# Kernel tuning notes

Hardware: AMD Instinct MI355X
Metric: run time of the kernel (lower is better)

Reference implementation:

```python
import jax, jax.numpy as jnp
import numpy as np

N = 100000
E = 1600000
IN_C, HID_C, OUT_C = 512, 256, 64
K = 10
ALPHA = 0.1


def setup_inputs() -> dict:
    key = jax.random.key(0)
    k1, k2, k3, k4 = jax.random.split(key, 4)
    x = jax.random.normal(k1, (N, IN_C), dtype=jnp.float32)
    edge_index = jax.random.randint(k2, (2, E), 0, N, dtype=jnp.int64)
    # Glorot-ish scaled linear weights
    W1 = jax.random.normal(k3, (HID_C, IN_C), dtype=jnp.float32) / np.sqrt(IN_C)
    b1 = jnp.zeros((HID_C,), dtype=jnp.float32)
    W2 = jax.random.normal(k4, (OUT_C, HID_C), dtype=jnp.float32) / np.sqrt(HID_C)
    b2 = jnp.zeros((OUT_C,), dtype=jnp.float32)
    # PPR init: temp[k] = alpha*(1-alpha)^k, temp[K] = (1-alpha)^K
    temp = ALPHA * (1.0 - ALPHA) ** np.arange(K + 1)
    temp[-1] = (1.0 - ALPHA) ** K
    temp = jnp.asarray(temp, dtype=jnp.float32)
    return {"x": x, "edge_index": edge_index, "W1": W1, "b1": b1,
            "W2": W2, "b2": b2, "temp": temp}


def _gcn_norm(edge_index, num_nodes):
    # add self loops with weight 1, symmetric normalization D^-1/2 A D^-1/2
    loop = jnp.arange(num_nodes, dtype=edge_index.dtype)
    src = jnp.concatenate([edge_index[0], loop])
    dst = jnp.concatenate([edge_index[1], loop])
    w = jnp.ones(src.shape[0], dtype=jnp.float32)
    deg = jax.ops.segment_sum(w, dst, num_segments=num_nodes)
    dinv = jnp.where(deg > 0, jax.lax.rsqrt(deg), 0.0)
    norm = dinv[src] * w * dinv[dst]
    return src, dst, norm


def reference(x, edge_index, W1, b1, W2, b2, temp):
    # MLP (inference mode: dropout is identity)
    h = jax.nn.relu(x @ W1.T + b1)
    h = h @ W2.T + b2  # [N, OUT_C]

    src, dst, norm = _gcn_norm(edge_index, N)
    norm = norm[:, None]

    def step(carry, gamma):
        xk, hidden = carry
        xk = jax.ops.segment_sum(norm * xk[src], dst, num_segments=N)
        hidden = hidden + gamma * xk
        return (xk, hidden), None

    hidden0 = temp[0] * h
    (_, hidden), _ = jax.lax.scan(step, (h, hidden0), temp[1:])
    return hidden
```

## Files before the change

### kernel.cpp

```cpp
#include <hip/hip_runtime.h>

#define IN_C   512
#define HID_C  256
#define OUT_C  64
#define KSTEPS 10

typedef __attribute__((ext_vector_type(8))) short bf16x8;
typedef __attribute__((ext_vector_type(4))) float f32x4;

__device__ __forceinline__ uint f2bf(float f) {
    uint u = __float_as_uint(f);
    return (u + 0x7fffu + ((u >> 16) & 1u)) >> 16;
}
__device__ __forceinline__ float bfl(uint u) { return __uint_as_float(u << 16); }
__device__ __forceinline__ float bfh(uint u) { return __uint_as_float(u & 0xffff0000u); }

__global__ void k_init(int* __restrict__ a, int* __restrict__ b, int n) {
    int i = blockIdx.x * blockDim.x + threadIdx.x;
    if (i < n) { a[i] = 0; b[i] = 0; }
}

__global__ void k_hist(const int* __restrict__ ei, int* __restrict__ cnt, int E) {
    int e = blockIdx.x * blockDim.x + threadIdx.x;
    if (e < E) atomicAdd(&cnt[ei[E + e]], 1);
}

__global__ void k_dinv(const int* __restrict__ cnt, float* __restrict__ dinv, int n) {
    int i = blockIdx.x * blockDim.x + threadIdx.x;
    if (i < n) dinv[i] = rsqrtf((float)cnt[i] + 1.0f);
}

__global__ void k_scan1(const int* __restrict__ cnt, int* __restrict__ ptr,
                        int* __restrict__ bsum, int n) {
    __shared__ int sh[256];
    int i = blockIdx.x * 256 + threadIdx.x;
    int v = (i < n) ? cnt[i] : 0;
    sh[threadIdx.x] = v;
    __syncthreads();
    for (int off = 1; off < 256; off <<= 1) {
        int t = (threadIdx.x >= off) ? sh[threadIdx.x - off] : 0;
        __syncthreads();
        sh[threadIdx.x] += t;
        __syncthreads();
    }
    if (i < n) ptr[i + 1] = sh[threadIdx.x];
    if (threadIdx.x == 255) bsum[blockIdx.x] = sh[255];
}

__global__ void k_scan2(int* __restrict__ bsum, int nb) {
    __shared__ int sh[512];
    int t = threadIdx.x;
    int v = (t < nb) ? bsum[t] : 0;
    sh[t] = v;
    __syncthreads();
    for (int off = 1; off < 512; off <<= 1) {
        int u = (t >= off) ? sh[t - off] : 0;
        __syncthreads();
        sh[t] += u;
        __syncthreads();
    }
    int ex = (t == 0) ? 0 : sh[t - 1];
    if (t < nb) bsum[t] = ex;
}

__global__ void k_scan3(int* __restrict__ ptr, const int* __restrict__ bsum, int n) {
    int i = blockIdx.x * blockDim.x + threadIdx.x;
    if (i < n) ptr[i + 1] += bsum[i >> 8];
    if (i == 0) ptr[0] = 0;
}

__global__ void k_scatter(const int* __restrict__ ei, const float* __restrict__ dinv,
                          const int* __restrict__ rowptr, int* __restrict__ fill,
                          int2* __restrict__ edges, int E) {
    int e = blockIdx.x * blockDim.x + threadIdx.x;
    if (e < E) {
        int s = ei[e], d = ei[E + e];
        float nv = dinv[s] * dinv[d];
        int pos = rowptr[d] + atomicAdd(&fill[d], 1);
        edges[pos] = make_int2(s, __float_as_int(nv));
    }
}

__global__ void k_cvtw1(const float* __restrict__ W1, ushort* __restrict__ w1kt) {
    int i = blockIdx.x * blockDim.x + threadIdx.x;
    if (i < HID_C * IN_C) {
        int o = i >> 9;
        int c = i & 511;
        int kb = c >> 3, j = c & 7;
        w1kt[((size_t)kb * HID_C + o) * 8 + j] = (ushort)f2bf(W1[i]);
    }
}

__global__ void k_cvtw2(const float* __restrict__ W2, ushort* __restrict__ w2kt) {
    int i = blockIdx.x * blockDim.x + threadIdx.x;
    if (i < OUT_C * HID_C) {
        int o = i >> 8, c = i & 255;
        int kb = c >> 3, j = c & 7;
        w2kt[((size_t)(kb * 64 + o)) * 8 + j] = (ushort)f2bf(W2[i]);
    }
}

__global__ __launch_bounds__(256, 4) void k_mlp(
    const float* __restrict__ x, const ushort* __restrict__ w1kt,
    const float* __restrict__ b1, const ushort* __restrict__ w2kt,
    const float* __restrict__ b2, const float* __restrict__ temp,
    ushort* __restrict__ h, float* __restrict__ out, int n)
{
    __shared__ uint4 smem4[2048];
    char* smem = (char*)smem4;

    const int tid = threadIdx.x;
    const int lane = tid & 63;
    const int w    = tid >> 6;
    const int l15  = lane & 15;
    const int l4   = lane >> 4;
    const int row0 = blockIdx.x * 64;

    f32x4 acc[4][4];
#pragma unroll
    for (int i = 0; i < 4; ++i)
#pragma unroll
        for (int j = 0; j < 4; ++j) acc[i][j] = (f32x4){0.f, 0.f, 0.f, 0.f};

    for (int k0 = 0; k0 < IN_C; k0 += 64) {
#pragma unroll
        for (int it = 0; it < 4; ++it) {
            int f  = tid + it * 256;
            int r  = f >> 4, c4 = f & 15;
            int gr = row0 + r; if (gr >= n) gr = n - 1;
            float4 v = *(const float4*)(x + (size_t)gr * IN_C + k0 + c4 * 4);
            uint p0 = f2bf(v.x) | (f2bf(v.y) << 16);
            uint p1 = f2bf(v.z) | (f2bf(v.w) << 16);
            int boff = (c4 * 8) ^ ((r & 7) << 4);
            *(uint2*)(smem + r * 128 + boff) = make_uint2(p0, p1);
        }
        __syncthreads();

#pragma unroll
        for (int kk = 0; kk < 2; ++kk) {
            bf16x8 af[4], bfr[4];
            int kb = kk * 4 + l4;
#pragma unroll
            for (int rf = 0; rf < 4; ++rf) {
                int r = rf * 16 + l15;
                af[rf] = *(const bf16x8*)(smem + r * 128 + ((kb ^ (r & 7)) << 4));
            }
            int kbg = (k0 >> 3) + kb;
#pragma unroll
            for (int nf = 0; nf < 4; ++nf) {
                int nn = w * 64 + nf * 16 + l15;
                bfr[nf] = *(const bf16x8*)(w1kt + ((size_t)kbg * HID_C + nn) * 8);
            }
#pragma unroll
            for (int rf = 0; rf < 4; ++rf)
#pragma unroll
                for (int nf = 0; nf < 4; ++nf)
                    acc[rf][nf] = __builtin_amdgcn_mfma_f32_16x16x32_bf16(
                        af[rf], bfr[nf], acc[rf][nf], 0, 0, 0);
        }
        __syncthreads();
    }

    float bias1[4];
#pragma unroll
    for (int nf = 0; nf < 4; ++nf) bias1[nf] = b1[w * 64 + nf * 16 + l15];
#pragma unroll
    for (int rf = 0; rf < 4; ++rf)
#pragma unroll
        for (int nf = 0; nf < 4; ++nf)
#pragma unroll
            for (int j = 0; j < 4; ++j) {
                int r = rf * 16 + l4 * 4 + j;
                int c = w * 64 + nf * 16 + l15;
                float v = fmaxf(acc[rf][nf][j] + bias1[nf], 0.f);
                int byte = r * 512 + ((((c >> 3) ^ (r & 7))) << 4) + (c & 7) * 2;
                *(ushort*)(smem + byte) = (ushort)f2bf(v);
            }
    __syncthreads();

    f32x4 acc2[4];
#pragma unroll
    for (int nf = 0; nf < 4; ++nf) acc2[nf] = (f32x4){0.f, 0.f, 0.f, 0.f};
#pragma unroll
    for (int kk = 0; kk < 8; ++kk) {
        int r = w * 16 + l15;
        int kb = kk * 4 + l4;
        bf16x8 a = *(const bf16x8*)(smem + r * 512 + ((kb ^ (r & 7)) << 4));
#pragma unroll
        for (int nf = 0; nf < 4; ++nf) {
            bf16x8 bb = *(const bf16x8*)(w2kt + ((size_t)kb * 64 + nf * 16 + l15) * 8);
            acc2[nf] = __builtin_amdgcn_mfma_f32_16x16x32_bf16(a, bb, acc2[nf], 0, 0, 0);
        }
    }

    float t0 = temp[0];
#pragma unroll
    for (int nf = 0; nf < 4; ++nf) {
        int c = nf * 16 + l15;
        float bias = b2[c];
#pragma unroll
        for (int j = 0; j < 4; ++j) {
            int gr = row0 + w * 16 + l4 * 4 + j;
            if (gr < n) {
                float v = acc2[nf][j] + bias;
                h[(size_t)gr * OUT_C + c]   = (ushort)f2bf(v);
                out[(size_t)gr * OUT_C + c] = t0 * v;
            }
        }
    }
}

__global__ __launch_bounds__(256) void k_prop(
    const int* __restrict__ rowptr, const int2* __restrict__ edges,
    const ushort* __restrict__ cur, ushort* __restrict__ nxt,
    float* __restrict__ out, const float* __restrict__ dinv,
    const float* __restrict__ temp, int kcur, int do_rmw, int do_nxt, int n)
{
    const int lane = threadIdx.x & 63;
    const int g    = lane >> 3;
    const int sl   = lane & 7;
    const int wid  = (blockIdx.x * blockDim.x + threadIdx.x) >> 6;
    const int nw   = (gridDim.x * blockDim.x) >> 6;
    const float gc = temp[kcur];
    const float gp = temp[kcur - 1];

    for (int base = wid * 8; base < n; base += nw * 8) {
        int d = base + g;
        bool act = d < n;
        int dd = act ? d : (n - 1);
        int b = rowptr[dd];
        int en = act ? rowptr[dd + 1] : b;
        float di = dinv[dd];
        size_t rowoff = (size_t)dd * OUT_C + sl * 8;

        uint4 sraw = *(const uint4*)(cur + rowoff);
        float c0 = bfl(sraw.x), c1 = bfh(sraw.x), c2 = bfl(sraw.y), c3 = bfh(sraw.y),
              c4 = bfl(sraw.z), c5 = bfh(sraw.z), c6 = bfl(sraw.w), c7 = bfh(sraw.w);
        float s = di * di;
        float a0 = s * c0, a1 = s * c1, a2 = s * c2, a3 = s * c3,
              a4 = s * c4, a5 = s * c5, a6 = s * c6, a7 = s * c7;

        int i = b;
        for (; i + 4 <= en; i += 4) {
            int2 e0 = edges[i], e1 = edges[i + 1], e2 = edges[i + 2], e3 = edges[i + 3];
            uint4 r0 = *(const uint4*)(cur + (size_t)e0.x * OUT_C + sl * 8);
            uint4 r1 = *(const uint4*)(cur + (size_t)e1.x * OUT_C + sl * 8);
            uint4 r2 = *(const uint4*)(cur + (size_t)e2.x * OUT_C + sl * 8);
            uint4 r3 = *(const uint4*)(cur + (size_t)e3.x * OUT_C + sl * 8);
            float w0 = __int_as_float(e0.y), w1 = __int_as_float(e1.y);
            float w2 = __int_as_float(e2.y), w3 = __int_as_float(e3.y);
            a0 = fmaf(w0, bfl(r0.x), a0); a1 = fmaf(w0, bfh(r0.x), a1);
            a2 = fmaf(w0, bfl(r0.y), a2); a3 = fmaf(w0, bfh(r0.y), a3);
            a4 = fmaf(w0, bfl(r0.z), a4); a5 = fmaf(w0, bfh(r0.z), a5);
            a6 = fmaf(w0, bfl(r0.w), a6); a7 = fmaf(w0, bfh(r0.w), a7);
            a0 = fmaf(w1, bfl(r1.x), a0); a1 = fmaf(w1, bfh(r1.x), a1);
            a2 = fmaf(w1, bfl(r1.y), a2); a3 = fmaf(w1, bfh(r1.y), a3);
            a4 = fmaf(w1, bfl(r1.z), a4); a5 = fmaf(w1, bfh(r1.z), a5);
            a6 = fmaf(w1, bfl(r1.w), a6); a7 = fmaf(w1, bfh(r1.w), a7);
            a0 = fmaf(w2, bfl(r2.x), a0); a1 = fmaf(w2, bfh(r2.x), a1);
            a2 = fmaf(w2, bfl(r2.y), a2); a3 = fmaf(w2, bfh(r2.y), a3);
            a4 = fmaf(w2, bfl(r2.z), a4); a5 = fmaf(w2, bfh(r2.z), a5);
            a6 = fmaf(w2, bfl(r2.w), a6); a7 = fmaf(w2, bfh(r2.w), a7);
            a0 = fmaf(w3, bfl(r3.x), a0); a1 = fmaf(w3, bfh(r3.x), a1);
            a2 = fmaf(w3, bfl(r3.y), a2); a3 = fmaf(w3, bfh(r3.y), a3);
            a4 = fmaf(w3, bfl(r3.z), a4); a5 = fmaf(w3, bfh(r3.z), a5);
            a6 = fmaf(w3, bfl(r3.w), a6); a7 = fmaf(w3, bfh(r3.w), a7);
        }
        for (; i < en; ++i) {
            int2 e = edges[i];
            uint4 r0 = *(const uint4*)(cur + (size_t)e.x * OUT_C + sl * 8);
            float w0 = __int_as_float(e.y);
            a0 = fmaf(w0, bfl(r0.x), a0); a1 = fmaf(w0, bfh(r0.x), a1);
            a2 = fmaf(w0, bfl(r0.y), a2); a3 = fmaf(w0, bfh(r0.y), a3);
            a4 = fmaf(w0, bfl(r0.z), a4); a5 = fmaf(w0, bfh(r0.z), a5);
            a6 = fmaf(w0, bfl(r0.w), a6); a7 = fmaf(w0, bfh(r0.w), a7);
        }

        if (act) {
            if (do_nxt) {
                uint4 pk;
                pk.x = f2bf(a0) | (f2bf(a1) << 16);
                pk.y = f2bf(a2) | (f2bf(a3) << 16);
                pk.z = f2bf(a4) | (f2bf(a5) << 16);
                pk.w = f2bf(a6) | (f2bf(a7) << 16);
                *(uint4*)(nxt + rowoff) = pk;
            }
            if (do_rmw) {
                float4* op = (float4*)(out + rowoff);
                float4 v0 = op[0], v1 = op[1];
                v0.x += gp * c0 + gc * a0; v0.y += gp * c1 + gc * a1;
                v0.z += gp * c2 + gc * a2; v0.w += gp * c3 + gc * a3;
                v1.x += gp * c4 + gc * a4; v1.y += gp * c5 + gc * a5;
                v1.z += gp * c6 + gc * a6; v1.w += gp * c7 + gc * a7;
                op[0] = v0; op[1] = v1;
            }
        }
    }
}

extern "C" void kernel_launch(void* const* d_in, const int* in_sizes, int n_in,
                              void* d_out, int out_size, void* d_ws, size_t ws_size,
                              hipStream_t stream)
{
    const float* x    = (const float*)d_in[0];
    const int*   ei   = (const int*)d_in[1];
    const float* W1   = (const float*)d_in[2];
    const float* b1   = (const float*)d_in[3];
    const float* W2   = (const float*)d_in[4];
    const float* b2   = (const float*)d_in[5];
    const float* temp = (const float*)d_in[6];
    float* out = (float*)d_out;

    const int N = in_sizes[0] / IN_C;
    const int E = in_sizes[1] / 2;

    char* ws = (char*)d_ws;
    ushort* bufA  = (ushort*)ws;
    ushort* bufB  = bufA + (size_t)N * OUT_C;
    int2*   edges = (int2*)(bufB + (size_t)N * OUT_C);
    ushort* w1kt  = (ushort*)(edges + E);
    ushort* w2kt  = w1kt + HID_C * IN_C;
    float*  dinv  = (float*)(w2kt + OUT_C * HID_C);
    int*    cnt    = (int*)(dinv + N);
    int*    fill   = cnt + N;
    int*    rowptr = fill + N;
    int*    bsum   = rowptr + (N + 16);

    const int nbN = (N + 255) / 256;
    const int nbE = (E + 255) / 256;

    k_init   <<<nbN, 256, 0, stream>>>(cnt, fill, N);
    k_hist   <<<nbE, 256, 0, stream>>>(ei, cnt, E);
    k_dinv   <<<nbN, 256, 0, stream>>>(cnt, dinv, N);
    k_scan1  <<<nbN, 256, 0, stream>>>(cnt, rowptr, bsum, N);
    k_scan2  <<<1,   512, 0, stream>>>(bsum, nbN);
    k_scan3  <<<nbN, 256, 0, stream>>>(rowptr, bsum, N);
    k_scatter<<<nbE, 256, 0, stream>>>(ei, dinv, rowptr, fill, edges, E);
    k_cvtw1  <<<(HID_C * IN_C + 255) / 256, 256, 0, stream>>>(W1, w1kt);
    k_cvtw2  <<<(OUT_C * HID_C + 255) / 256, 256, 0, stream>>>(W2, w2kt);

    k_mlp<<<(N + 63) / 64, 256, 0, stream>>>(x, w1kt, b1, w2kt, b2, temp, bufA, out, N);

    ushort* cur = bufA;
    ushort* nxt = bufB;
    for (int k = 1; k <= KSTEPS; ++k) {
        int do_rmw = (k % 2 == 0) ? 1 : 0;
        int do_nxt = (k < KSTEPS) ? 1 : 0;
        k_prop<<<2048, 256, 0, stream>>>(rowptr, edges, cur, nxt, out, dinv,
                                         temp, k, do_rmw, do_nxt, N);
        ushort* t = cur; cur = nxt; nxt = t;
    }
}
```

Measured before the change: 589.7 us.

## Split feature matrix into four 16-column planes to shrink gather working set

The MLP output is stored as four column planes of 16 bf16 features each, and the propagation kernel walks the planes one at a time so each gather touches a 3.2MB plane instead of the full 12.8MB matrix, aiming for better cache hit rates on random neighbor reads. Each node is now handled by 4 lanes loading 8 bytes apiece, and the grid grows to one block per 64 nodes. In exchange, CSR row pointers and edge lists are read four times per step, each gather moves only 8 bytes per lane, and the out read-modify-write is split into strided 16-byte pieces.

```diff
diff --git a/kernel.cpp b/kernel.cpp
--- a/kernel.cpp
+++ b/kernel.cpp
@@ -115,6 +115,7 @@
     const int l15  = lane & 15;
     const int l4   = lane >> 4;
     const int row0 = blockIdx.x * 64;
+    const size_t plane = (size_t)n * 16;
 
     f32x4 acc[4][4];
 #pragma unroll
@@ -203,7 +204,7 @@
             int gr = row0 + w * 16 + l4 * 4 + j;
             if (gr < n) {
                 float v = acc2[nf][j] + bias;
-                h[(size_t)gr * OUT_C + c]   = (ushort)f2bf(v);
+                h[(size_t)nf * plane + (size_t)gr * 16 + l15] = (ushort)f2bf(v);
                 out[(size_t)gr * OUT_C + c] = t0 * v;
             }
         }
@@ -217,82 +218,66 @@
     const float* __restrict__ temp, int kcur, int do_rmw, int do_nxt, int n)
 {
     const int lane = threadIdx.x & 63;
-    const int g    = lane >> 3;
-    const int sl   = lane & 7;
+    const int g    = lane >> 2;
+    const int q    = lane & 3;
     const int wid  = (blockIdx.x * blockDim.x + threadIdx.x) >> 6;
     const int nw   = (gridDim.x * blockDim.x) >> 6;
     const float gc = temp[kcur];
     const float gp = temp[kcur - 1];
-
-    for (int base = wid * 8; base < n; base += nw * 8) {
-        int d = base + g;
-        bool act = d < n;
-        int dd = act ? d : (n - 1);
-        int b = rowptr[dd];
-        int en = act ? rowptr[dd + 1] : b;
-        float di = dinv[dd];
-        size_t rowoff = (size_t)dd * OUT_C + sl * 8;
-
-        uint4 sraw = *(const uint4*)(cur + rowoff);
-        float c0 = bfl(sraw.x), c1 = bfh(sraw.x), c2 = bfl(sraw.y), c3 = bfh(sraw.y),
-              c4 = bfl(sraw.z), c5 = bfh(sraw.z), c6 = bfl(sraw.w), c7 = bfh(sraw.w);
-        float s = di * di;
-        float a0 = s * c0, a1 = s * c1, a2 = s * c2, a3 = s * c3,
-              a4 = s * c4, a5 = s * c5, a6 = s * c6, a7 = s * c7;
-
-        int i = b;
-        for (; i + 4 <= en; i += 4) {
-            int2 e0 = edges[i], e1 = edges[i + 1], e2 = edges[i + 2], e3 = edges[i + 3];
-            uint4 r0 = *(const uint4*)(cur + (size_t)e0.x * OUT_C + sl * 8);
-            uint4 r1 = *(const uint4*)(cur + (size_t)e1.x * OUT_C + sl * 8);
-            uint4 r2 = *(const uint4*)(cur + (size_t)e2.x * OUT_C + sl * 8);
-            uint4 r3 = *(const uint4*)(cur + (size_t)e3.x * OUT_C + sl * 8);
-            float w0 = __int_as_float(e0.y), w1 = __int_as_float(e1.y);
-            float w2 = __int_as_float(e2.y), w3 = __int_as_float(e3.y);
-            a0 = fmaf(w0, bfl(r0.x), a0); a1 = fmaf(w0, bfh(r0.x), a1);
-            a2 = fmaf(w0, bfl(r0.y), a2); a3 = fmaf(w0, bfh(r0.y), a3);
-            a4 = fmaf(w0, bfl(r0.z), a4); a5 = fmaf(w0, bfh(r0.z), a5);
-            a6 = fmaf(w0, bfl(r0.w), a6); a7 = fmaf(w0, bfh(r0.w), a7);
-            a0 = fmaf(w1, bfl(r1.x), a0); a1 = fmaf(w1, bfh(r1.x), a1);
-            a2 = fmaf(w1, bfl(r1.y), a2); a3 = fmaf(w1, bfh(r1.y), a3);
-            a4 = fmaf(w1, bfl(r1.z), a4); a5 = fmaf(w1, bfh(r1.z), a5);
-            a6 = fmaf(w1, bfl(r1.w), a6); a7 = fmaf(w1, bfh(r1.w), a7);
-            a0 = fmaf(w2, bfl(r2.x), a0); a1 = fmaf(w2, bfh(r2.x), a1);
-            a2 = fmaf(w2, bfl(r2.y), a2); a3 = fmaf(w2, bfh(r2.y), a3);
-            a4 = fmaf(w2, bfl(r2.z), a4); a5 = fmaf(w2, bfh(r2.z), a5);
-            a6 = fmaf(w2, bfl(r2.w), a6); a7 = fmaf(w2, bfh(r2.w), a7);
-            a0 = fmaf(w3, bfl(r3.x), a0); a1 = fmaf(w3, bfh(r3.x), a1);
-            a2 = fmaf(w3, bfl(r3.y), a2); a3 = fmaf(w3, bfh(r3.y), a3);
-            a4 = fmaf(w3, bfl(r3.z), a4); a5 = fmaf(w3, bfh(r3.z), a5);
-            a6 = fmaf(w3, bfl(r3.w), a6); a7 = fmaf(w3, bfh(r3.w), a7);
-        }
-        for (; i < en; ++i) {
-            int2 e = edges[i];
-            uint4 r0 = *(const uint4*)(cur + (size_t)e.x * OUT_C + sl * 8);
-            float w0 = __int_as_float(e.y);
-            a0 = fmaf(w0, bfl(r0.x), a0); a1 = fmaf(w0, bfh(r0.x), a1);
-            a2 = fmaf(w0, bfl(r0.y), a2); a3 = fmaf(w0, bfh(r0.y), a3);
-            a4 = fmaf(w0, bfl(r0.z), a4); a5 = fmaf(w0, bfh(r0.z), a5);
-            a6 = fmaf(w0, bfl(r0.w), a6); a7 = fmaf(w0, bfh(r0.w), a7);
-        }
-
-        if (act) {
-            if (do_nxt) {
-                uint4 pk;
-                pk.x = f2bf(a0) | (f2bf(a1) << 16);
-                pk.y = f2bf(a2) | (f2bf(a3) << 16);
-                pk.z = f2bf(a4) | (f2bf(a5) << 16);
-                pk.w = f2bf(a6) | (f2bf(a7) << 16);
-                *(uint4*)(nxt + rowoff) = pk;
-            }
-            if (do_rmw) {
-                float4* op = (float4*)(out + rowoff);
-                float4 v0 = op[0], v1 = op[1];
-                v0.x += gp * c0 + gc * a0; v0.y += gp * c1 + gc * a1;
-                v0.z += gp * c2 + gc * a2; v0.w += gp * c3 + gc * a3;
-                v1.x += gp * c4 + gc * a4; v1.y += gp * c5 + gc * a5;
-                v1.z += gp * c6 + gc * a6; v1.w += gp * c7 + gc * a7;
-                op[0] = v0; op[1] = v1;
+    const size_t plane = (size_t)n * 16;
+
+    for (int p = 0; p < 4; ++p) {
+        const ushort* curp = cur + (size_t)p * plane;
+        ushort*       nxtp = nxt + (size_t)p * plane;
+
+        for (int base = wid * 16; base < n; base += nw * 16) {
+            int d = base + g;
+            bool act = d < n;
+            int dd = act ? d : (n - 1);
+            int b = rowptr[dd];
+            int en = act ? rowptr[dd + 1] : b;
+            float di = dinv[dd];
+            size_t ro = (size_t)dd * 16 + q * 4;
+
+            uint2 sraw = *(const uint2*)(curp + ro);
+            float c0 = bfl(sraw.x), c1 = bfh(sraw.x);
+            float c2 = bfl(sraw.y), c3 = bfh(sraw.y);
+            float s = di * di;
+            float a0 = s * c0, a1 = s * c1, a2 = s * c2, a3 = s * c3;
+
+            int i = b;
+            for (; i + 2 <= en; i += 2) {
+                int2 e0 = edges[i], e1 = edges[i + 1];
+                uint2 r0 = *(const uint2*)(curp + (size_t)e0.x * 16 + q * 4);
+                uint2 r1 = *(const uint2*)(curp + (size_t)e1.x * 16 + q * 4);
+                float w0 = __int_as_float(e0.y), w1 = __int_as_float(e1.y);
+                a0 = fmaf(w0, bfl(r0.x), a0); a1 = fmaf(w0, bfh(r0.x), a1);
+                a2 = fmaf(w0, bfl(r0.y), a2); a3 = fmaf(w0, bfh(r0.y), a3);
+                a0 = fmaf(w1, bfl(r1.x), a0); a1 = fmaf(w1, bfh(r1.x), a1);
+                a2 = fmaf(w1, bfl(r1.y), a2); a3 = fmaf(w1, bfh(r1.y), a3);
+            }
+            if (i < en) {
+                int2 e0 = edges[i];
+                uint2 r0 = *(const uint2*)(curp + (size_t)e0.x * 16 + q * 4);
+                float w0 = __int_as_float(e0.y);
+                a0 = fmaf(w0, bfl(r0.x), a0); a1 = fmaf(w0, bfh(r0.x), a1);
+                a2 = fmaf(w0, bfl(r0.y), a2); a3 = fmaf(w0, bfh(r0.y), a3);
+            }
+
+            if (act) {
+                if (do_nxt) {
+                    uint2 pk;
+                    pk.x = f2bf(a0) | (f2bf(a1) << 16);
+                    pk.y = f2bf(a2) | (f2bf(a3) << 16);
+                    *(uint2*)(nxtp + ro) = pk;
+                }
+                if (do_rmw) {
+                    float4* op = (float4*)(out + (size_t)dd * OUT_C + p * 16 + q * 4);
+                    float4 v = op[0];
+                    v.x += gp * c0 + gc * a0; v.y += gp * c1 + gc * a1;
+                    v.z += gp * c2 + gc * a2; v.w += gp * c3 + gc * a3;
+                    op[0] = v;
+                }
             }
         }
     }
@@ -328,6 +313,7 @@
 
     const int nbN = (N + 255) / 256;
     const int nbE = (E + 255) / 256;
+    const int nbP = (N + 63) / 64;
 
     k_init   <<<nbN, 256, 0, stream>>>(cnt, fill, N);
     k_hist   <<<nbE, 256, 0, stream>>>(ei, cnt, E);
@@ -346,8 +332,8 @@
     for (int k = 1; k <= KSTEPS; ++k) {
         int do_rmw = (k % 2 == 0) ? 1 : 0;
         int do_nxt = (k < KSTEPS) ? 1 : 0;
-        k_prop<<<2048, 256, 0, stream>>>(rowptr, edges, cur, nxt, out, dinv,
-                                         temp, k, do_rmw, do_nxt, N);
+        k_prop<<<nbP, 256, 0, stream>>>(rowptr, edges, cur, nxt, out, dinv,
+                                        temp, k, do_rmw, do_nxt, N);
         ushort* t = cur; cur = nxt; nxt = t;
     }
 }
```

Result: slower. 993.2 us (+68.4%).

## Sort destination nodes by degree and launch one 8-lane group per node

Applied to the files above, without the earlier changes.

Adds a small counting sort that buckets nodes by in-degree, capped at 63, into a permutation array. The propagation kernel then gives each 8-lane group exactly one node taken from that permutation, with a grid sized to cover all nodes instead of a fixed 2048-block grid-stride loop. The aim is to cut load imbalance inside a wavefront, since the 8 groups in a wave now have similar edge counts. In exchange, rows are visited in permuted order, so writes to nxt and out lose their coalescing and locality, and three extra setup kernels run.

```diff
diff --git a/kernel.cpp b/kernel.cpp
--- a/kernel.cpp
+++ b/kernel.cpp
@@ -81,6 +81,28 @@
     }
 }
 
+__global__ void k_dhist(const int* __restrict__ cnt, int* __restrict__ dh, int n) {
+    int i = blockIdx.x * blockDim.x + threadIdx.x;
+    if (i < n) atomicAdd(&dh[min(cnt[i], 63)], 1);
+}
+
+__global__ void k_dscan(int* __restrict__ dh) {
+    if (threadIdx.x == 0) {
+        int acc = 0;
+        for (int b = 0; b < 64; ++b) { int v = dh[b]; dh[b] = acc; acc += v; }
+    }
+}
+
+__global__ void k_dscat(const int* __restrict__ cnt, const int* __restrict__ dh,
+                        int* __restrict__ dfill, int* __restrict__ perm, int n) {
+    int i = blockIdx.x * blockDim.x + threadIdx.x;
+    if (i < n) {
+        int b = min(cnt[i], 63);
+        int pos = dh[b] + atomicAdd(&dfill[b], 1);
+        perm[pos] = i;
+    }
+}
+
 __global__ void k_cvtw1(const float* __restrict__ W1, ushort* __restrict__ w1kt) {
     int i = blockIdx.x * blockDim.x + threadIdx.x;
     if (i < HID_C * IN_C) {
@@ -212,6 +234,7 @@
 
 __global__ __launch_bounds__(256) void k_prop(
     const int* __restrict__ rowptr, const int2* __restrict__ edges,
+    const int* __restrict__ perm,
     const ushort* __restrict__ cur, ushort* __restrict__ nxt,
     float* __restrict__ out, const float* __restrict__ dinv,
     const float* __restrict__ temp, int kcur, int do_rmw, int do_nxt, int n)
@@ -220,80 +243,77 @@
     const int g    = lane >> 3;
     const int sl   = lane & 7;
     const int wid  = (blockIdx.x * blockDim.x + threadIdx.x) >> 6;
-    const int nw   = (gridDim.x * blockDim.x) >> 6;
     const float gc = temp[kcur];
     const float gp = temp[kcur - 1];
 
-    for (int base = wid * 8; base < n; base += nw * 8) {
-        int d = base + g;
-        bool act = d < n;
-        int dd = act ? d : (n - 1);
-        int b = rowptr[dd];
-        int en = act ? rowptr[dd + 1] : b;
-        float di = dinv[dd];
-        size_t rowoff = (size_t)dd * OUT_C + sl * 8;
-
-        uint4 sraw = *(const uint4*)(cur + rowoff);
-        float c0 = bfl(sraw.x), c1 = bfh(sraw.x), c2 = bfl(sraw.y), c3 = bfh(sraw.y),
-              c4 = bfl(sraw.z), c5 = bfh(sraw.z), c6 = bfl(sraw.w), c7 = bfh(sraw.w);
-        float s = di * di;
-        float a0 = s * c0, a1 = s * c1, a2 = s * c2, a3 = s * c3,
-              a4 = s * c4, a5 = s * c5, a6 = s * c6, a7 = s * c7;
-
-        int i = b;
-        for (; i + 4 <= en; i += 4) {
-            int2 e0 = edges[i], e1 = edges[i + 1], e2 = edges[i + 2], e3 = edges[i + 3];
-            uint4 r0 = *(const uint4*)(cur + (size_t)e0.x * OUT_C + sl * 8);
-            uint4 r1 = *(const uint4*)(cur + (size_t)e1.x * OUT_C + sl * 8);
-            uint4 r2 = *(const uint4*)(cur + (size_t)e2.x * OUT_C + sl * 8);
-            uint4 r3 = *(const uint4*)(cur + (size_t)e3.x * OUT_C + sl * 8);
-            float w0 = __int_as_float(e0.y), w1 = __int_as_float(e1.y);
-            float w2 = __int_as_float(e2.y), w3 = __int_as_float(e3.y);
-            a0 = fmaf(w0, bfl(r0.x), a0); a1 = fmaf(w0, bfh(r0.x), a1);
-            a2 = fmaf(w0, bfl(r0.y), a2); a3 = fmaf(w0, bfh(r0.y), a3);
-            a4 = fmaf(w0, bfl(r0.z), a4); a5 = fmaf(w0, bfh(r0.z), a5);
-            a6 = fmaf(w0, bfl(r0.w), a6); a7 = fmaf(w0, bfh(r0.w), a7);
-            a0 = fmaf(w1, bfl(r1.x), a0); a1 = fmaf(w1, bfh(r1.x), a1);
-            a2 = fmaf(w1, bfl(r1.y), a2); a3 = fmaf(w1, bfh(r1.y), a3);
-            a4 = fmaf(w1, bfl(r1.z), a4); a5 = fmaf(w1, bfh(r1.z), a5);
-            a6 = fmaf(w1, bfl(r1.w), a6); a7 = fmaf(w1, bfh(r1.w), a7);
-            a0 = fmaf(w2, bfl(r2.x), a0); a1 = fmaf(w2, bfh(r2.x), a1);
-            a2 = fmaf(w2, bfl(r2.y), a2); a3 = fmaf(w2, bfh(r2.y), a3);
-            a4 = fmaf(w2, bfl(r2.z), a4); a5 = fmaf(w2, bfh(r2.z), a5);
-            a6 = fmaf(w2, bfl(r2.w), a6); a7 = fmaf(w2, bfh(r2.w), a7);
-            a0 = fmaf(w3, bfl(r3.x), a0); a1 = fmaf(w3, bfh(r3.x), a1);
-            a2 = fmaf(w3, bfl(r3.y), a2); a3 = fmaf(w3, bfh(r3.y), a3);
-            a4 = fmaf(w3, bfl(r3.z), a4); a5 = fmaf(w3, bfh(r3.z), a5);
-            a6 = fmaf(w3, bfl(r3.w), a6); a7 = fmaf(w3, bfh(r3.w), a7);
-        }
-        for (; i < en; ++i) {
-            int2 e = edges[i];
-            uint4 r0 = *(const uint4*)(cur + (size_t)e.x * OUT_C + sl * 8);
-            float w0 = __int_as_float(e.y);
-            a0 = fmaf(w0, bfl(r0.x), a0); a1 = fmaf(w0, bfh(r0.x), a1);
-            a2 = fmaf(w0, bfl(r0.y), a2); a3 = fmaf(w0, bfh(r0.y), a3);
-            a4 = fmaf(w0, bfl(r0.z), a4); a5 = fmaf(w0, bfh(r0.z), a5);
-            a6 = fmaf(w0, bfl(r0.w), a6); a7 = fmaf(w0, bfh(r0.w), a7);
-        }
-
-        if (act) {
-            if (do_nxt) {
-                uint4 pk;
-                pk.x = f2bf(a0) | (f2bf(a1) << 16);
-                pk.y = f2bf(a2) | (f2bf(a3) << 16);
-                pk.z = f2bf(a4) | (f2bf(a5) << 16);
-                pk.w = f2bf(a6) | (f2bf(a7) << 16);
-                *(uint4*)(nxt + rowoff) = pk;
-            }
-            if (do_rmw) {
-                float4* op = (float4*)(out + rowoff);
-                float4 v0 = op[0], v1 = op[1];
-                v0.x += gp * c0 + gc * a0; v0.y += gp * c1 + gc * a1;
-                v0.z += gp * c2 + gc * a2; v0.w += gp * c3 + gc * a3;
-                v1.x += gp * c4 + gc * a4; v1.y += gp * c5 + gc * a5;
-                v1.z += gp * c6 + gc * a6; v1.w += gp * c7 + gc * a7;
-                op[0] = v0; op[1] = v1;
-            }
+    int slot = wid * 8 + g;
+    bool act = slot < n;
+    int dd = perm[act ? slot : (n - 1)];
+    int b = rowptr[dd];
+    int en = act ? rowptr[dd + 1] : b;
+    float di = dinv[dd];
+    size_t rowoff = (size_t)dd * OUT_C + sl * 8;
+
+    uint4 sraw = *(const uint4*)(cur + rowoff);
+    float c0 = bfl(sraw.x), c1 = bfh(sraw.x), c2 = bfl(sraw.y), c3 = bfh(sraw.y),
+          c4 = bfl(sraw.z), c5 = bfh(sraw.z), c6 = bfl(sraw.w), c7 = bfh(sraw.w);
+    float s = di * di;
+    float a0 = s * c0, a1 = s * c1, a2 = s * c2, a3 = s * c3,
+          a4 = s * c4, a5 = s * c5, a6 = s * c6, a7 = s * c7;
+
+    int i = b;
+    for (; i + 4 <= en; i += 4) {
+        int2 e0 = edges[i], e1 = edges[i + 1], e2 = edges[i + 2], e3 = edges[i + 3];
+        uint4 r0 = *(const uint4*)(cur + (size_t)e0.x * OUT_C + sl * 8);
+        uint4 r1 = *(const uint4*)(cur + (size_t)e1.x * OUT_C + sl * 8);
+        uint4 r2 = *(const uint4*)(cur + (size_t)e2.x * OUT_C + sl * 8);
+        uint4 r3 = *(const uint4*)(cur + (size_t)e3.x * OUT_C + sl * 8);
+        float w0 = __int_as_float(e0.y), w1 = __int_as_float(e1.y);
+        float w2 = __int_as_float(e2.y), w3 = __int_as_float(e3.y);
+        a0 = fmaf(w0, bfl(r0.x), a0); a1 = fmaf(w0, bfh(r0.x), a1);
+        a2 = fmaf(w0, bfl(r0.y), a2); a3 = fmaf(w0, bfh(r0.y), a3);
+        a4 = fmaf(w0, bfl(r0.z), a4); a5 = fmaf(w0, bfh(r0.z), a5);
+        a6 = fmaf(w0, bfl(r0.w), a6); a7 = fmaf(w0, bfh(r0.w), a7);
+        a0 = fmaf(w1, bfl(r1.x), a0); a1 = fmaf(w1, bfh(r1.x), a1);
+        a2 = fmaf(w1, bfl(r1.y), a2); a3 = fmaf(w1, bfh(r1.y), a3);
+        a4 = fmaf(w1, bfl(r1.z), a4); a5 = fmaf(w1, bfh(r1.z), a5);
+        a6 = fmaf(w1, bfl(r1.w), a6); a7 = fmaf(w1, bfh(r1.w), a7);
+        a0 = fmaf(w2, bfl(r2.x), a0); a1 = fmaf(w2, bfh(r2.x), a1);
+        a2 = fmaf(w2, bfl(r2.y), a2); a3 = fmaf(w2, bfh(r2.y), a3);
+        a4 = fmaf(w2, bfl(r2.z), a4); a5 = fmaf(w2, bfh(r2.z), a5);
+        a6 = fmaf(w2, bfl(r2.w), a6); a7 = fmaf(w2, bfh(r2.w), a7);
+        a0 = fmaf(w3, bfl(r3.x), a0); a1 = fmaf(w3, bfh(r3.x), a1);
+        a2 = fmaf(w3, bfl(r3.y), a2); a3 = fmaf(w3, bfh(r3.y), a3);
+        a4 = fmaf(w3, bfl(r3.z), a4); a5 = fmaf(w3, bfh(r3.z), a5);
+        a6 = fmaf(w3, bfl(r3.w), a6); a7 = fmaf(w3, bfh(r3.w), a7);
+    }
+    for (; i < en; ++i) {
+        int2 e = edges[i];
+        uint4 r0 = *(const uint4*)(cur + (size_t)e.x * OUT_C + sl * 8);
+        float w0 = __int_as_float(e.y);
+        a0 = fmaf(w0, bfl(r0.x), a0); a1 = fmaf(w0, bfh(r0.x), a1);
+        a2 = fmaf(w0, bfl(r0.y), a2); a3 = fmaf(w0, bfh(r0.y), a3);
+        a4 = fmaf(w0, bfl(r0.z), a4); a5 = fmaf(w0, bfh(r0.z), a5);
+        a6 = fmaf(w0, bfl(r0.w), a6); a7 = fmaf(w0, bfh(r0.w), a7);
+    }
+
+    if (act) {
+        if (do_nxt) {
+            uint4 pk;
+            pk.x = f2bf(a0) | (f2bf(a1) << 16);
+            pk.y = f2bf(a2) | (f2bf(a3) << 16);
+            pk.z = f2bf(a4) | (f2bf(a5) << 16);
+            pk.w = f2bf(a6) | (f2bf(a7) << 16);
+            *(uint4*)(nxt + rowoff) = pk;
+        }
+        if (do_rmw) {
+            float4* op = (float4*)(out + rowoff);
+            float4 v0 = op[0], v1 = op[1];
+            v0.x += gp * c0 + gc * a0; v0.y += gp * c1 + gc * a1;
+            v0.z += gp * c2 + gc * a2; v0.w += gp * c3 + gc * a3;
+            v1.x += gp * c4 + gc * a4; v1.y += gp * c5 + gc * a5;
+            v1.z += gp * c6 + gc * a6; v1.w += gp * c7 + gc * a7;
+            op[0] = v0; op[1] = v1;
         }
     }
 }
@@ -325,17 +345,25 @@
     int*    fill   = cnt + N;
     int*    rowptr = fill + N;
     int*    bsum   = rowptr + (N + 16);
+    int*    perm   = bsum + 512;
+    int*    dh     = perm + N;
+    int*    dfill  = dh + 64;
 
     const int nbN = (N + 255) / 256;
     const int nbE = (E + 255) / 256;
+    const int nbP = (N + 31) / 32;
 
     k_init   <<<nbN, 256, 0, stream>>>(cnt, fill, N);
+    k_init   <<<1,    64, 0, stream>>>(dh, dfill, 64);
     k_hist   <<<nbE, 256, 0, stream>>>(ei, cnt, E);
     k_dinv   <<<nbN, 256, 0, stream>>>(cnt, dinv, N);
     k_scan1  <<<nbN, 256, 0, stream>>>(cnt, rowptr, bsum, N);
     k_scan2  <<<1,   512, 0, stream>>>(bsum, nbN);
     k_scan3  <<<nbN, 256, 0, stream>>>(rowptr, bsum, N);
     k_scatter<<<nbE, 256, 0, stream>>>(ei, dinv, rowptr, fill, edges, E);
+    k_dhist  <<<nbN, 256, 0, stream>>>(cnt, dh, N);
+    k_dscan  <<<1,    64, 0, stream>>>(dh);
+    k_dscat  <<<nbN, 256, 0, stream>>>(cnt, dh, dfill, perm, N);
     k_cvtw1  <<<(HID_C * IN_C + 255) / 256, 256, 0, stream>>>(W1, w1kt);
     k_cvtw2  <<<(OUT_C * HID_C + 255) / 256, 256, 0, stream>>>(W2, w2kt);
 
@@ -346,8 +374,8 @@
     for (int k = 1; k <= KSTEPS; ++k) {
         int do_rmw = (k % 2 == 0) ? 1 : 0;
         int do_nxt = (k < KSTEPS) ? 1 : 0;
-        k_prop<<<2048, 256, 0, stream>>>(rowptr, edges, cur, nxt, out, dinv,
-                                         temp, k, do_rmw, do_nxt, N);
+        k_prop<<<nbP, 256, 0, stream>>>(rowptr, edges, perm, cur, nxt, out, dinv,
+                                        temp, k, do_rmw, do_nxt, N);
         ushort* t = cur; cur = nxt; nxt = t;
     }
 }
```

After: 1.047 ms. 77.5% more time.
